# Performance work log

Hardware: AMD Instinct MI355X
Metric: run time of the kernel (lower is better)

The kernel has to match this reference:

```python
import jax, jax.numpy as jnp
import numpy as np

B, L, D, N = 32, 2048, 1024, 16
N_ITERS = 4
EPS = 1e-8
RMS_EPS = 1e-6
H = 2 * D  # SwiGLU hidden


def setup_inputs() -> dict:
    key = jax.random.key(0)
    ks = jax.random.split(key, 16)
    w = lambda i, shape: jax.random.normal(ks[i], shape, dtype=jnp.float32) * 0.02
    return {
        "encoder_output": jax.random.normal(ks[0], (B, L, D), dtype=jnp.float32),
        "slots_noise": jax.random.normal(ks[1], (B, N, D), dtype=jnp.float32),
        "slots_mu": w(2, (1, 1, D)),
        "slots_sigma": jnp.abs(w(3, (1, 1, D))),
        "g_in": jnp.ones((D,), jnp.float32),     # norm_input.weight
        "g_slots": jnp.ones((D,), jnp.float32),  # norm_slots.weight
        "Wq": w(4, (D, D)),   # torch Linear weight layout (out, in)
        "Wk": w(5, (D, D)),
        "Wv": w(6, (D, D)),
        "w1": w(7, (H, D)),
        "w2": w(8, (H, D)),
        "w3": w(9, (D, H)),
        "W_ih": w(10, (3 * D, D)),  # GRUCell weight_ih (r,z,n stacked)
        "W_hh": w(11, (3 * D, D)),
        "b_ih": jnp.zeros((3 * D,), jnp.float32),
        "b_hh": jnp.zeros((3 * D,), jnp.float32),
    }


def _rmsnorm(x, g):
    var = jnp.mean(x * x, axis=-1, keepdims=True)
    return x * jax.lax.rsqrt(var + RMS_EPS) * g


def _gru_cell(x, h, W_ih, W_hh, b_ih, b_hh):
    # torch.nn.GRUCell: gates ordered (r, z, n)
    gi = x @ W_ih.T + b_ih   # [..., 3D]
    gh = h @ W_hh.T + b_hh
    gi_r, gi_z, gi_n = jnp.split(gi, 3, axis=-1)
    gh_r, gh_z, gh_n = jnp.split(gh, 3, axis=-1)
    r = jax.nn.sigmoid(gi_r + gh_r)
    z = jax.nn.sigmoid(gi_z + gh_z)
    n = jnp.tanh(gi_n + r * gh_n)
    return (1.0 - z) * n + z * h


def reference(encoder_output, slots_noise, slots_mu, slots_sigma, g_in, g_slots,
              Wq, Wk, Wv, w1, w2, w3, W_ih, W_hh, b_ih, b_hh):
    d = encoder_output.shape[-1]
    scale = d ** (-0.5)

    inputs = _rmsnorm(encoder_output, g_in)          # [B, L, D]
    k = inputs @ Wk.T                                # [B, L, D]
    v = inputs @ Wv.T                                # [B, L, D]

    slots = slots_mu + slots_sigma * slots_noise     # [B, N, D]

    for _ in range(N_ITERS):
        slots_prev = slots
        s = _rmsnorm(slots, g_slots)                 # [B, N, D]
        q = s @ Wq.T                                 # [B, N, D]
        dots = jnp.einsum('bnd,bld->bnl', q, k) * scale   # [B, N, L]
        attn = jax.nn.softmax(dots, axis=1)          # competitive softmax over slots
        updates = jnp.einsum('bnl,bld->bnd', attn + EPS, v)     # [B, N, D]
        updates = updates / (jnp.sum(attn, axis=-1, keepdims=True) + EPS)
        # SwiGLU
        updates = (jax.nn.silu(updates @ w1.T) * (updates @ w2.T)) @ w3.T
        slots = _gru_cell(updates, slots_prev, W_ih, W_hh, b_ih, b_hh)
    return slots
```

## Files before the change

kernel.cpp:

```cpp
#include <hip/hip_runtime.h>
#include <hip/hip_bf16.h>
#include <stdint.h>


typedef __bf16 bf16;
typedef __bf16 bf16x2 __attribute__((ext_vector_type(2)));
typedef __bf16 bf16x4 __attribute__((ext_vector_type(4)));
typedef __bf16 bf16x8 __attribute__((ext_vector_type(8)));
typedef float  f32x4  __attribute__((ext_vector_type(4)));

#define MFMA16(a,b,c) __builtin_amdgcn_mfma_f32_16x16x32_bf16((a),(b),(c),0,0,0)

__device__ __forceinline__ void gload16(const void* g, void* l) {
  __builtin_amdgcn_global_load_lds((__attribute__((address_space(1))) const void*)g,
                                   (__attribute__((address_space(3))) void*)l, 16, 0, 0);
}

template<int OUT_F32>
__global__ __launch_bounds__(256, 4)
void gemm_bt64(const bf16* __restrict__ A0, const bf16* __restrict__ B0, void* __restrict__ C0,
               const bf16* __restrict__ A1, const bf16* __restrict__ B1, void* __restrict__ C1,
               int N, int K)
{
  const bf16* A = blockIdx.z ? A1 : A0;
  const bf16* B = blockIdx.z ? B1 : B0;
  void* C = blockIdx.z ? C1 : C0;
  __shared__ __align__(16) bf16 As[64 * 64];
  __shared__ __align__(16) bf16 Bs[64 * 64];
  const int tid = threadIdx.x, wave = tid >> 6, lane = tid & 63;
  const int wm = wave >> 1, wn = wave & 1;
  const int brow = blockIdx.y * 64, bcol = blockIdx.x * 64;
  const int r8 = lane >> 3, c8 = (lane & 7) * 8;
  const int cl = lane & 15, rh = lane >> 4;
  f32x4 acc[2][2] = {};

  for (int k0 = 0; k0 < K; k0 += 64) {
    __syncthreads();
    gload16(A + (size_t)(brow + wave * 16 + r8) * K + k0 + c8,     &As[(wave * 16) * 64]);
    gload16(A + (size_t)(brow + wave * 16 + 8 + r8) * K + k0 + c8, &As[(wave * 16 + 8) * 64]);
    gload16(B + (size_t)(bcol + wave * 16 + r8) * K + k0 + c8,     &Bs[(wave * 16) * 64]);
    gload16(B + (size_t)(bcol + wave * 16 + 8 + r8) * K + k0 + c8, &Bs[(wave * 16 + 8) * 64]);
    __syncthreads();
#pragma unroll
    for (int kk = 0; kk < 2; ++kk) {
      bf16x8 af[2], bfv[2];
#pragma unroll
      for (int m = 0; m < 2; ++m)
        af[m] = *(const bf16x8*)&As[(wm * 32 + m * 16 + cl) * 64 + kk * 32 + rh * 8];
#pragma unroll
      for (int n = 0; n < 2; ++n)
        bfv[n] = *(const bf16x8*)&Bs[(wn * 32 + n * 16 + cl) * 64 + kk * 32 + rh * 8];
#pragma unroll
      for (int m = 0; m < 2; ++m)
#pragma unroll
        for (int n = 0; n < 2; ++n)
          acc[m][n] = MFMA16(af[m], bfv[n], acc[m][n]);
    }
  }
#pragma unroll
  for (int m = 0; m < 2; ++m)
#pragma unroll
    for (int n = 0; n < 2; ++n) {
      int row0 = brow + wm * 32 + m * 16 + rh * 4;
      int col  = bcol + wn * 32 + n * 16 + cl;
#pragma unroll
      for (int r = 0; r < 4; ++r) {
        if (OUT_F32) ((float*)C)[(size_t)(row0 + r) * N + col] = acc[m][n][r];
        else         ((bf16*)C)[(size_t)(row0 + r) * N + col] = (bf16)acc[m][n][r];
      }
    }
}

__global__ __launch_bounds__(256, 4)
void gemm_swiglu(const bf16* __restrict__ A, const bf16* __restrict__ B12, bf16* __restrict__ G)
{
  __shared__ __align__(16) bf16 As[64 * 64];
  __shared__ __align__(16) bf16 B1s[64 * 64];
  __shared__ __align__(16) bf16 B2s[64 * 64];
  const int tid = threadIdx.x, wave = tid >> 6, lane = tid & 63;
  const int wm = wave >> 1, wn = wave & 1;
  const int brow = blockIdx.y * 64, bcol = blockIdx.x * 64;
  const int r8 = lane >> 3, c8 = (lane & 7) * 8;
  const int cl = lane & 15, rh = lane >> 4;
  f32x4 acc1[2][2] = {}, acc2[2][2] = {};

  for (int k0 = 0; k0 < 1024; k0 += 64) {
    __syncthreads();
    gload16(A   + (size_t)(brow + wave * 16 + r8) * 1024 + k0 + c8,            &As[(wave * 16) * 64]);
    gload16(A   + (size_t)(brow + wave * 16 + 8 + r8) * 1024 + k0 + c8,        &As[(wave * 16 + 8) * 64]);
    gload16(B12 + (size_t)(bcol + wave * 16 + r8) * 1024 + k0 + c8,            &B1s[(wave * 16) * 64]);
    gload16(B12 + (size_t)(bcol + wave * 16 + 8 + r8) * 1024 + k0 + c8,        &B1s[(wave * 16 + 8) * 64]);
    gload16(B12 + (size_t)(2048 + bcol + wave * 16 + r8) * 1024 + k0 + c8,     &B2s[(wave * 16) * 64]);
    gload16(B12 + (size_t)(2048 + bcol + wave * 16 + 8 + r8) * 1024 + k0 + c8, &B2s[(wave * 16 + 8) * 64]);
    __syncthreads();
#pragma unroll
    for (int kk = 0; kk < 2; ++kk) {
      bf16x8 af[2], b1v[2], b2v[2];
#pragma unroll
      for (int m = 0; m < 2; ++m)
        af[m] = *(const bf16x8*)&As[(wm * 32 + m * 16 + cl) * 64 + kk * 32 + rh * 8];
#pragma unroll
      for (int n = 0; n < 2; ++n) {
        b1v[n] = *(const bf16x8*)&B1s[(wn * 32 + n * 16 + cl) * 64 + kk * 32 + rh * 8];
        b2v[n] = *(const bf16x8*)&B2s[(wn * 32 + n * 16 + cl) * 64 + kk * 32 + rh * 8];
      }
#pragma unroll
      for (int m = 0; m < 2; ++m)
#pragma unroll
        for (int n = 0; n < 2; ++n) {
          acc1[m][n] = MFMA16(af[m], b1v[n], acc1[m][n]);
          acc2[m][n] = MFMA16(af[m], b2v[n], acc2[m][n]);
        }
    }
  }
#pragma unroll
  for (int m = 0; m < 2; ++m)
#pragma unroll
    for (int n = 0; n < 2; ++n) {
      int row0 = brow + wm * 32 + m * 16 + rh * 4;
      int col  = bcol + wn * 32 + n * 16 + cl;
#pragma unroll
      for (int r = 0; r < 4; ++r) {
        float h1 = acc1[m][n][r], h2 = acc2[m][n][r];
        G[(size_t)(row0 + r) * 2048 + col] = (bf16)(h1 / (1.f + __expf(-h1)) * h2);
      }
    }
}

__global__ __launch_bounds__(256, 2)
void fused_attn(const bf16* __restrict__ qm, const bf16* __restrict__ x,
                float* __restrict__ part, float* __restrict__ attn_sum)
{
  const int lc = blockIdx.x, b = blockIdx.y;
  const int tid = threadIdx.x, wave = tid >> 6, lane = tid & 63;
  const int cl = lane & 15, rh = lane >> 4;
  __shared__ __align__(16) bf16 ss[16 * 1024];
  __shared__ __align__(16) bf16 ks[128 * 64];
  __shared__ __align__(16) float p_lds[128 * 20];

  const bf16* sb = qm + (size_t)b * 16 * 1024;
#pragma unroll
  for (int i = 0; i < 8; ++i)
    gload16(sb + i * 2048 + tid * 8, &ss[i * 2048 + wave * 512]);

  const bf16* kb = x + ((size_t)b * 2048 + lc * 128) * 1024;
  f32x4 acc[2] = {};
  for (int kt = 0; kt < 16; ++kt) {
    __syncthreads();
#pragma unroll
    for (int i = 0; i < 4; ++i) {
      int row = i * 32 + wave * 8 + (lane >> 3);
      gload16(kb + (size_t)row * 1024 + kt * 64 + (lane & 7) * 8, &ks[(i * 32 + wave * 8) * 64]);
    }
    __syncthreads();
#pragma unroll
    for (int kk = 0; kk < 2; ++kk) {
      bf16x8 af = *(const bf16x8*)&ss[cl * 1024 + kt * 64 + kk * 32 + rh * 8];
#pragma unroll
      for (int n = 0; n < 2; ++n) {
        bf16x8 bfv = *(const bf16x8*)&ks[(wave * 32 + n * 16 + cl) * 64 + kk * 32 + rh * 8];
        acc[n] = MFMA16(af, bfv, acc[n]);
      }
    }
  }
  const float scale = 0.03125f;
  float rs[4] = {0.f, 0.f, 0.f, 0.f};
#pragma unroll
  for (int n = 0; n < 2; ++n) {
    float xv[4];
#pragma unroll
    for (int r = 0; r < 4; ++r) xv[r] = acc[n][r] * scale;
    float mx = fmaxf(fmaxf(xv[0], xv[1]), fmaxf(xv[2], xv[3]));
    mx = fmaxf(mx, __shfl_xor(mx, 16));
    mx = fmaxf(mx, __shfl_xor(mx, 32));
    float e[4], sm = 0.f;
#pragma unroll
    for (int r = 0; r < 4; ++r) { e[r] = __expf(xv[r] - mx); sm += e[r]; }
    sm += __shfl_xor(sm, 16);
    sm += __shfl_xor(sm, 32);
    float inv = 1.f / sm;
    f32x4 pk;
#pragma unroll
    for (int r = 0; r < 4; ++r) { float av = e[r] * inv; rs[r] += av; pk[r] = av; }
    int ll = wave * 32 + n * 16 + cl;
    *(f32x4*)&p_lds[ll * 20 + rh * 4] = pk;
  }
#pragma unroll
  for (int off = 1; off < 16; off <<= 1) {
#pragma unroll
    for (int r = 0; r < 4; ++r) rs[r] += __shfl_xor(rs[r], off);
  }
  if (cl == 0) {
#pragma unroll
    for (int r = 0; r < 4; ++r) atomicAdd(&attn_sum[b * 16 + rh * 4 + r], rs[r]);
  }
  __syncthreads();

  const bf16* vb = x + ((size_t)b * 2048 + lc * 128) * 1024 + tid * 4;
  float pacc[16][4] = {};
  for (int l = 0; l < 128; ++l) {
    bf16x4 vv = *(const bf16x4*)(vb + (size_t)l * 1024);
    float vf0 = (float)vv[0], vf1 = (float)vv[1], vf2 = (float)vv[2], vf3 = (float)vv[3];
    float pv[16];
    *(f32x4*)&pv[0]  = *(const f32x4*)&p_lds[l * 20];
    *(f32x4*)&pv[4]  = *(const f32x4*)&p_lds[l * 20 + 4];
    *(f32x4*)&pv[8]  = *(const f32x4*)&p_lds[l * 20 + 8];
    *(f32x4*)&pv[12] = *(const f32x4*)&p_lds[l * 20 + 12];
#pragma unroll
    for (int n = 0; n < 16; ++n) {
      pacc[n][0] += pv[n] * vf0; pacc[n][1] += pv[n] * vf1;
      pacc[n][2] += pv[n] * vf2; pacc[n][3] += pv[n] * vf3;
    }
  }
  float* pb = part + ((size_t)(lc * 32 + b) * 16) * 1024 + tid * 4;
#pragma unroll
  for (int n = 0; n < 16; ++n)
    *(f32x4*)(pb + (size_t)n * 1024) = *(f32x4*)&pacc[n][0];
}

__global__ void updates_finalize(const float* __restrict__ part, const float* __restrict__ attn_sum,
                                 bf16* __restrict__ updraw)
{
  int idx = blockIdx.x * 256 + threadIdx.x;
  int m = idx >> 10;
  float sm = 0.f;
#pragma unroll
  for (int ls = 0; ls < 16; ++ls) sm += part[idx + (size_t)ls * 524288];
  updraw[idx] = (bf16)(sm / (attn_sum[m] + 1e-8f));
}

__global__ __launch_bounds__(256)
void gru_pw_fused(const float* __restrict__ gi, const float* __restrict__ gh,
                  const float* __restrict__ bih, const float* __restrict__ bhh,
                  const float* __restrict__ g_sl,
                  float* __restrict__ slots, bf16* __restrict__ slots_bf,
                  bf16* __restrict__ s_bf, float* __restrict__ outp)
{
  const int m = blockIdx.x, tid = threadIdx.x;
  const int d0 = tid * 4;
  const size_t base = (size_t)m * 3072 + d0;
  f32x4 gir = *(const f32x4*)(gi + base),        ghr = *(const f32x4*)(gh + base);
  f32x4 giz = *(const f32x4*)(gi + base + 1024), ghz = *(const f32x4*)(gh + base + 1024);
  f32x4 gin = *(const f32x4*)(gi + base + 2048), ghn = *(const f32x4*)(gh + base + 2048);
  f32x4 br  = *(const f32x4*)(bih + d0),        bhr = *(const f32x4*)(bhh + d0);
  f32x4 bz  = *(const f32x4*)(bih + 1024 + d0), bhz = *(const f32x4*)(bhh + 1024 + d0);
  f32x4 bn  = *(const f32x4*)(bih + 2048 + d0), bhn = *(const f32x4*)(bhh + 2048 + d0);
  f32x4 h   = *(const f32x4*)(slots + (size_t)m * 1024 + d0);
  float o[4]; float ssum = 0.f;
#pragma unroll
  for (int j = 0; j < 4; ++j) {
    float r  = gir[j] + br[j] + ghr[j] + bhr[j];
    float z  = giz[j] + bz[j] + ghz[j] + bhz[j];
    float nn = gin[j] + bn[j];
    float hn = ghn[j] + bhn[j];
    r = 1.f / (1.f + expf(-r));
    z = 1.f / (1.f + expf(-z));
    nn = tanhf(nn + r * hn);
    o[j] = (1.f - z) * nn + z * h[j];
    ssum += o[j] * o[j];
  }
#pragma unroll
  for (int off = 32; off; off >>= 1) ssum += __shfl_xor(ssum, off);
  __shared__ float red[4];
  if ((tid & 63) == 0) red[tid >> 6] = ssum;
  __syncthreads();
  float tot = red[0] + red[1] + red[2] + red[3];
  float rsc = rsqrtf(tot * (1.f / 1024.f) + 1e-6f);
  f32x4 gv = *(const f32x4*)(g_sl + d0);
  f32x4 of; bf16x4 ob, sb;
#pragma unroll
  for (int j = 0; j < 4; ++j) { of[j] = o[j]; ob[j] = (bf16)o[j]; sb[j] = (bf16)(o[j] * rsc * gv[j]); }
  *(f32x4*)(slots + (size_t)m * 1024 + d0) = of;
  *(f32x4*)(outp  + (size_t)m * 1024 + d0) = of;
  *(bf16x4*)(slots_bf + (size_t)m * 1024 + d0) = ob;
  *(bf16x4*)(s_bf     + (size_t)m * 1024 + d0) = sb;
}

__global__ __launch_bounds__(256)
void init_slots_fused(const float* __restrict__ noise, const float* __restrict__ mu,
                      const float* __restrict__ sigma, const float* __restrict__ g_sl,
                      float* __restrict__ slots, bf16* __restrict__ slots_bf,
                      bf16* __restrict__ s_bf)
{
  const int m = blockIdx.x, tid = threadIdx.x;
  const int d0 = tid * 4;
  f32x4 nz = *(const f32x4*)(noise + (size_t)m * 1024 + d0);
  f32x4 mv = *(const f32x4*)(mu + d0);
  f32x4 sg = *(const f32x4*)(sigma + d0);
  float o[4]; float ssum = 0.f;
#pragma unroll
  for (int j = 0; j < 4; ++j) { o[j] = mv[j] + sg[j] * nz[j]; ssum += o[j] * o[j]; }
#pragma unroll
  for (int off = 32; off; off >>= 1) ssum += __shfl_xor(ssum, off);
  __shared__ float red[4];
  if ((tid & 63) == 0) red[tid >> 6] = ssum;
  __syncthreads();
  float tot = red[0] + red[1] + red[2] + red[3];
  float rsc = rsqrtf(tot * (1.f / 1024.f) + 1e-6f);
  f32x4 gv = *(const f32x4*)(g_sl + d0);
  f32x4 of; bf16x4 ob, sb;
#pragma unroll
  for (int j = 0; j < 4; ++j) { of[j] = o[j]; ob[j] = (bf16)o[j]; sb[j] = (bf16)(o[j] * rsc * gv[j]); }
  *(f32x4*)(slots + (size_t)m * 1024 + d0) = of;
  *(bf16x4*)(slots_bf + (size_t)m * 1024 + d0) = ob;
  *(bf16x4*)(s_bf     + (size_t)m * 1024 + d0) = sb;
}

__global__ __launch_bounds__(256)
void rmsnorm_cast(const float* __restrict__ x, const float* __restrict__ g, bf16* __restrict__ y)
{
  const int row = blockIdx.x, tid = threadIdx.x;
  float4 xv = ((const float4*)(x + (size_t)row * 1024))[tid];
  float ss = xv.x * xv.x + xv.y * xv.y + xv.z * xv.z + xv.w * xv.w;
#pragma unroll
  for (int off = 32; off; off >>= 1) ss += __shfl_xor(ss, off);
  __shared__ float red[4];
  if ((tid & 63) == 0) red[tid >> 6] = ss;
  __syncthreads();
  float tot = red[0] + red[1] + red[2] + red[3];
  float rs = rsqrtf(tot * (1.f / 1024.f) + 1e-6f);
  float4 gv = ((const float4*)g)[tid];
  bf16x4 o;
  o[0] = (bf16)(xv.x * rs * gv.x); o[1] = (bf16)(xv.y * rs * gv.y);
  o[2] = (bf16)(xv.z * rs * gv.z); o[3] = (bf16)(xv.w * rs * gv.w);
  *(bf16x4*)(y + (size_t)row * 1024 + tid * 4) = o;
}

__global__ __launch_bounds__(256)
void transpose_cast(const float* __restrict__ in, bf16* __restrict__ out)
{
  __shared__ float tile[32][33];
  const int bx = blockIdx.x * 32, by = blockIdx.y * 32;
  const int tx = threadIdx.x & 31, ty = threadIdx.x >> 5;
#pragma unroll
  for (int i = 0; i < 32; i += 8)
    tile[ty + i][tx] = in[(size_t)(by + ty + i) * 1024 + bx + tx];
  __syncthreads();
#pragma unroll
  for (int i = 0; i < 32; i += 8)
    out[(size_t)(bx + ty + i) * 1024 + by + tx] = (bf16)tile[tx][ty + i];
}

__global__ void cast_bf16_x4(const float* __restrict__ x, bf16* __restrict__ y)
{
  int i = (blockIdx.x * 256 + threadIdx.x) * 4;
  float4 v = *(const float4*)(x + i);
  bf16x4 o; o[0] = (bf16)v.x; o[1] = (bf16)v.y; o[2] = (bf16)v.z; o[3] = (bf16)v.w;
  *(bf16x4*)(y + i) = o;
}

extern "C" void kernel_launch(void* const* d_in, const int* in_sizes, int n_in,
                              void* d_out, int out_size, void* d_ws, size_t ws_size,
                              hipStream_t stream)
{
  const float* enc    = (const float*)d_in[0];
  const float* noise  = (const float*)d_in[1];
  const float* mu     = (const float*)d_in[2];
  const float* sigma  = (const float*)d_in[3];
  const float* g_in   = (const float*)d_in[4];
  const float* g_sl   = (const float*)d_in[5];
  const float* Wq     = (const float*)d_in[6];
  const float* Wk     = (const float*)d_in[7];
  const float* Wv     = (const float*)d_in[8];
  const float* w1     = (const float*)d_in[9];
  const float* w2     = (const float*)d_in[10];
  const float* w3     = (const float*)d_in[11];
  const float* Wih    = (const float*)d_in[12];
  const float* Whh    = (const float*)d_in[13];
  const float* bih    = (const float*)d_in[14];
  const float* bhh    = (const float*)d_in[15];

  char* p = (char*)d_ws;
  auto alloc = [&](size_t bytes) { char* r = p; p += (bytes + 255) & ~(size_t)255; return (void*)r; };

  bf16* inputs  = (bf16*)alloc((size_t)32 * 2048 * 1024 * 2);
  bf16* qm_w    = (bf16*)alloc((size_t)1024 * 1024 * 2);
  bf16* wv_b    = (bf16*)alloc((size_t)1024 * 1024 * 2);
  bf16* wqT_b   = (bf16*)alloc((size_t)1024 * 1024 * 2);
  bf16* wkT_b   = (bf16*)alloc((size_t)1024 * 1024 * 2);
  bf16* w12_b   = (bf16*)alloc((size_t)4096 * 1024 * 2);
  bf16* w3_b    = (bf16*)alloc((size_t)1024 * 2048 * 2);
  bf16* wih_b   = (bf16*)alloc((size_t)3072 * 1024 * 2);
  bf16* whh_b   = (bf16*)alloc((size_t)3072 * 1024 * 2);
  float* slots  = (float*)alloc(512 * 1024 * 4);
  bf16* slots_bf= (bf16*)alloc(512 * 1024 * 2);
  bf16* s_bf    = (bf16*)alloc(512 * 1024 * 2);
  bf16* qm_bf   = (bf16*)alloc(512 * 1024 * 2);
  float* attn_sum = (float*)alloc(32 * 16 * 4);
  float* part   = (float*)alloc((size_t)16 * 512 * 1024 * 4);
  bf16* updraw  = (bf16*)alloc(512 * 1024 * 2);
  bf16* upd_bf  = (bf16*)alloc(512 * 1024 * 2);
  bf16* g_bf    = (bf16*)alloc((size_t)512 * 2048 * 2);
  bf16* swout   = (bf16*)alloc(512 * 1024 * 2);
  float* gif    = (float*)alloc((size_t)512 * 3072 * 4);
  float* ghf    = (float*)alloc((size_t)512 * 3072 * 4);

  transpose_cast<<<dim3(32, 32), 256, 0, stream>>>(Wq, wqT_b);
  transpose_cast<<<dim3(32, 32), 256, 0, stream>>>(Wk, wkT_b);
  gemm_bt64<0><<<dim3(16, 16, 1), 256, 0, stream>>>(wkT_b, wqT_b, qm_w, wkT_b, wqT_b, qm_w, 1024, 1024);
  cast_bf16_x4<<<1024, 256, 0, stream>>>(Wv, wv_b);
  cast_bf16_x4<<<2048, 256, 0, stream>>>(w1, w12_b);
  cast_bf16_x4<<<2048, 256, 0, stream>>>(w2, w12_b + (size_t)2048 * 1024);
  cast_bf16_x4<<<2048, 256, 0, stream>>>(w3, w3_b);
  cast_bf16_x4<<<3072, 256, 0, stream>>>(Wih, wih_b);
  cast_bf16_x4<<<3072, 256, 0, stream>>>(Whh, whh_b);

  rmsnorm_cast<<<65536, 256, 0, stream>>>(enc, g_in, inputs);
  init_slots_fused<<<512, 256, 0, stream>>>(noise, mu, sigma, g_sl, slots, slots_bf, s_bf);

  for (int it = 0; it < 4; ++it) {
    gemm_bt64<0><<<dim3(16, 8, 1), 256, 0, stream>>>(s_bf, qm_w, qm_bf, s_bf, qm_w, qm_bf, 1024, 1024);
    hipMemsetAsync(attn_sum, 0, 32 * 16 * 4, stream);
    fused_attn<<<dim3(16, 32), 256, 0, stream>>>(qm_bf, inputs, part, attn_sum);
    updates_finalize<<<2048, 256, 0, stream>>>(part, attn_sum, updraw);
    gemm_bt64<0><<<dim3(16, 8, 1), 256, 0, stream>>>(updraw, wv_b, upd_bf, updraw, wv_b, upd_bf, 1024, 1024);
    gemm_swiglu<<<dim3(32, 8), 256, 0, stream>>>(upd_bf, w12_b, g_bf);
    gemm_bt64<0><<<dim3(16, 8, 1), 256, 0, stream>>>(g_bf, w3_b, swout, g_bf, w3_b, swout, 1024, 2048);
    gemm_bt64<1><<<dim3(48, 8, 2), 256, 0, stream>>>(swout, wih_b, gif, slots_bf, whh_b, ghf, 3072, 1024);
    float* outp = (it == 3) ? (float*)d_out : slots;
    gru_pw_fused<<<512, 256, 0, stream>>>(gif, ghf, bih, bhh, g_sl, slots, slots_bf, s_bf, outp);
  }
}
```

Measured before the change: 784.2 us.

## Double-buffer and swizzle LDS in fused_attn, fold attn_sum zeroing into GEMM

The fused attention kernel now double-buffers the K tile in dynamic shared memory, issuing the next tile's global-to-LDS loads before computing the current one and waiting on a partial vmcnt. It also XOR-swizzles both the query and K LDS layouts to reduce bank conflicts. The separate hipMemsetAsync of attn_sum is removed, and the zeroing moves into the preceding q GEMM's first block. The larger LDS footprint (about 74KB) may reduce occupancy, and the hand-written waitcnt/barrier scheme must be correct for the async LDS loads.

```diff
diff --git a/kernel.cpp b/kernel.cpp
--- a/kernel.cpp
+++ b/kernel.cpp
@@ -20,8 +20,12 @@
 __global__ __launch_bounds__(256, 4)
 void gemm_bt64(const bf16* __restrict__ A0, const bf16* __restrict__ B0, void* __restrict__ C0,
                const bf16* __restrict__ A1, const bf16* __restrict__ B1, void* __restrict__ C1,
-               int N, int K)
-{
+               int N, int K, float* zbuf)
+{
+  if (zbuf != nullptr && blockIdx.x == 0 && blockIdx.y == 0 && blockIdx.z == 0) {
+    zbuf[threadIdx.x] = 0.f;
+    zbuf[threadIdx.x + 256] = 0.f;
+  }
   const bf16* A = blockIdx.z ? A1 : A0;
   const bf16* B = blockIdx.z ? B1 : B0;
   void* C = blockIdx.z ? C1 : C0;
@@ -131,38 +135,65 @@
 void fused_attn(const bf16* __restrict__ qm, const bf16* __restrict__ x,
                 float* __restrict__ part, float* __restrict__ attn_sum)
 {
+  extern __shared__ __align__(16) char smem[];
+  char* ss  = smem;
+  char* ksl = smem + 32768;
+  float* p_lds = (float*)(smem + 65536);
+
   const int lc = blockIdx.x, b = blockIdx.y;
   const int tid = threadIdx.x, wave = tid >> 6, lane = tid & 63;
   const int cl = lane & 15, rh = lane >> 4;
-  __shared__ __align__(16) bf16 ss[16 * 1024];
-  __shared__ __align__(16) bf16 ks[128 * 64];
-  __shared__ __align__(16) float p_lds[128 * 20];
 
   const bf16* sb = qm + (size_t)b * 16 * 1024;
-#pragma unroll
-  for (int i = 0; i < 8; ++i)
-    gload16(sb + i * 2048 + tid * 8, &ss[i * 2048 + wave * 512]);
+  {
+    const int c16 = tid & 127, row2 = tid >> 7;
+#pragma unroll
+    for (int i = 0; i < 8; ++i) {
+      int row = i * 2 + row2;
+      int colb = (c16 * 16) ^ ((row & 7) << 4);
+      gload16(sb + row * 1024 + colb / 2, ss + i * 4096 + wave * 1024);
+    }
+  }
 
   const bf16* kb = x + ((size_t)b * 2048 + lc * 128) * 1024;
+  const int ksw  = ((lane & 7) ^ ((lane >> 3) & 7)) * 8;
+  const int krow = wave * 8 + (lane >> 3);
+
+#define STAGE_KS(KT) {                                                            \
+    char* d_ = ksl + ((KT) & 1) * 16384;                                          \
+    _Pragma("unroll")                                                             \
+    for (int i = 0; i < 4; ++i)                                                   \
+      gload16(kb + (size_t)(i * 32 + krow) * 1024 + (KT) * 64 + ksw,              \
+              d_ + (i * 32 + wave * 8) * 128);                                    \
+  }
+
   f32x4 acc[2] = {};
+  STAGE_KS(0)
   for (int kt = 0; kt < 16; ++kt) {
-    __syncthreads();
-#pragma unroll
-    for (int i = 0; i < 4; ++i) {
-      int row = i * 32 + wave * 8 + (lane >> 3);
-      gload16(kb + (size_t)row * 1024 + kt * 64 + (lane & 7) * 8, &ks[(i * 32 + wave * 8) * 64]);
-    }
-    __syncthreads();
+    if (kt < 15) { STAGE_KS(kt + 1) }
+    __builtin_amdgcn_sched_barrier(0);
+    if (kt < 15) asm volatile("s_waitcnt vmcnt(4)" ::: "memory");
+    else         asm volatile("s_waitcnt vmcnt(0)" ::: "memory");
+    __builtin_amdgcn_sched_barrier(0);
+    __builtin_amdgcn_s_barrier();
+    const char* sbuf = ksl + (kt & 1) * 16384;
 #pragma unroll
     for (int kk = 0; kk < 2; ++kk) {
-      bf16x8 af = *(const bf16x8*)&ss[cl * 1024 + kt * 64 + kk * 32 + rh * 8];
+      bf16x8 af = *(const bf16x8*)(ss + cl * 2048 +
+                    ((kt * 128 + kk * 64 + rh * 16) ^ ((cl & 7) << 4)));
 #pragma unroll
       for (int n = 0; n < 2; ++n) {
-        bf16x8 bfv = *(const bf16x8*)&ks[(wave * 32 + n * 16 + cl) * 64 + kk * 32 + rh * 8];
+        int row = wave * 32 + n * 16 + cl;
+        bf16x8 bfv = *(const bf16x8*)(sbuf + row * 128 +
+                      ((kk * 64 + rh * 16) ^ ((row & 7) << 4)));
         acc[n] = MFMA16(af, bfv, acc[n]);
       }
     }
-  }
+    __builtin_amdgcn_s_barrier();
+    __builtin_amdgcn_sched_barrier(0);
+  }
+#undef STAGE_KS
+
   const float scale = 0.03125f;
   float rs[4] = {0.f, 0.f, 0.f, 0.f};
 #pragma unroll
@@ -397,7 +428,7 @@
 
   transpose_cast<<<dim3(32, 32), 256, 0, stream>>>(Wq, wqT_b);
   transpose_cast<<<dim3(32, 32), 256, 0, stream>>>(Wk, wkT_b);
-  gemm_bt64<0><<<dim3(16, 16, 1), 256, 0, stream>>>(wkT_b, wqT_b, qm_w, wkT_b, wqT_b, qm_w, 1024, 1024);
+  gemm_bt64<0><<<dim3(16, 16, 1), 256, 0, stream>>>(wkT_b, wqT_b, qm_w, wkT_b, wqT_b, qm_w, 1024, 1024, nullptr);
   cast_bf16_x4<<<1024, 256, 0, stream>>>(Wv, wv_b);
   cast_bf16_x4<<<2048, 256, 0, stream>>>(w1, w12_b);
   cast_bf16_x4<<<2048, 256, 0, stream>>>(w2, w12_b + (size_t)2048 * 1024);
@@ -408,15 +439,17 @@
   rmsnorm_cast<<<65536, 256, 0, stream>>>(enc, g_in, inputs);
   init_slots_fused<<<512, 256, 0, stream>>>(noise, mu, sigma, g_sl, slots, slots_bf, s_bf);
 
+  hipFuncSetAttribute(reinterpret_cast<const void*>(fused_attn),
+                      hipFuncAttributeMaxDynamicSharedMemorySize, 75776);
+
   for (int it = 0; it < 4; ++it) {
-    gemm_bt64<0><<<dim3(16, 8, 1), 256, 0, stream>>>(s_bf, qm_w, qm_bf, s_bf, qm_w, qm_bf, 1024, 1024);
-    hipMemsetAsync(attn_sum, 0, 32 * 16 * 4, stream);
-    fused_attn<<<dim3(16, 32), 256, 0, stream>>>(qm_bf, inputs, part, attn_sum);
+    gemm_bt64<0><<<dim3(16, 8, 1), 256, 0, stream>>>(s_bf, qm_w, qm_bf, s_bf, qm_w, qm_bf, 1024, 1024, attn_sum);
+    fused_attn<<<dim3(16, 32), 256, 75776, stream>>>(qm_bf, inputs, part, attn_sum);
     updates_finalize<<<2048, 256, 0, stream>>>(part, attn_sum, updraw);
-    gemm_bt64<0><<<dim3(16, 8, 1), 256, 0, stream>>>(updraw, wv_b, upd_bf, updraw, wv_b, upd_bf, 1024, 1024);
+    gemm_bt64<0><<<dim3(16, 8, 1), 256, 0, stream>>>(updraw, wv_b, upd_bf, updraw, wv_b, upd_bf, 1024, 1024, nullptr);
     gemm_swiglu<<<dim3(32, 8), 256, 0, stream>>>(upd_bf, w12_b, g_bf);
-    gemm_bt64<0><<<dim3(16, 8, 1), 256, 0, stream>>>(g_bf, w3_b, swout, g_bf, w3_b, swout, 1024, 2048);
-    gemm_bt64<1><<<dim3(48, 8, 2), 256, 0, stream>>>(swout, wih_b, gif, slots_bf, whh_b, ghf, 3072, 1024);
+    gemm_bt64<0><<<dim3(16, 8, 1), 256, 0, stream>>>(g_bf, w3_b, swout, g_bf, w3_b, swout, 1024, 2048, nullptr);
+    gemm_bt64<1><<<dim3(48, 8, 2), 256, 0, stream>>>(swout, wih_b, gif, slots_bf, whh_b, ghf, 3072, 1024, nullptr);
     float* outp = (it == 3) ? (float*)d_out : slots;
     gru_pw_fused<<<512, 256, 0, stream>>>(gif, ghf, bih, bhh, g_sl, slots, slots_bf, s_bf, outp);
   }
```

After: 796.6 us. Within noise of the previous version (+1.6%).
